# Performance work log

Hardware: AMD Instinct MI355X
Metric: run time of the kernel (lower is better)

Reference implementation:

```python
import jax, jax.numpy as jnp
import numpy as np

D_MODEL = 768
N_HEADS = 12
D_K = D_MODEL // N_HEADS
BATCH = 1
SEQ = 4096


def setup_inputs() -> dict:
    key = jax.random.key(0)
    kx, kq, kk, kv, ko = jax.random.split(key, 5)
    s = 1.0 / np.sqrt(D_MODEL)
    return {
        "x": jax.random.normal(kx, (BATCH, SEQ, D_MODEL), dtype=jnp.float32),
        "wq": jax.random.normal(kq, (D_MODEL, D_MODEL), dtype=jnp.float32) * s,
        "wk": jax.random.normal(kk, (D_MODEL, D_MODEL), dtype=jnp.float32) * s,
        "wv": jax.random.normal(kv, (D_MODEL, D_MODEL), dtype=jnp.float32) * s,
        "wo": jax.random.normal(ko, (D_MODEL, D_MODEL), dtype=jnp.float32) * s,
    }


def reference(x, wq, wk, wv, wo):
    B, S, D = x.shape
    H, dk = N_HEADS, D_K
    # nn.Linear(x) = x @ W.T ; reshape to [B,H,S,dk]
    def proj(w):
        return (x @ w.T).reshape(B, S, H, dk).transpose(0, 2, 1, 3)
    q, k, v = proj(wq), proj(wk), proj(wv)
    scores = jnp.einsum('bhqd,bhkd->bhqk', q, k) / np.sqrt(dk).astype(np.float32)
    attn = jax.nn.softmax(scores, axis=-1)
    out = jnp.einsum('bhqk,bhkd->bhqd', attn, v)
    out = out.transpose(0, 2, 1, 3).reshape(B, S, D)
    return out @ wo.T
```

## Files before the change

### kernel.cpp

```cpp
#include <hip/hip_runtime.h>
#include <stdint.h>

#define SEQ 4096
#define DMODEL 768
#define NHEADS 12
#define DKH 64

typedef __attribute__((ext_vector_type(8))) short short8;
typedef __attribute__((ext_vector_type(4))) float floatx4;

__device__ __forceinline__ unsigned short f2bf(float f) {
    unsigned int u = __float_as_uint(f);
    u += 0x7fffu + ((u >> 16) & 1u);
    return (unsigned short)(u >> 16);
}

__device__ __forceinline__ float exp2fast(float x) {
    return __builtin_amdgcn_exp2f(x);
}

__device__ __forceinline__ unsigned int cvt_pk_bf16(float lo, float hi) {
    unsigned int r;
    asm("v_cvt_pk_bf16_f32 %0, %1, %2" : "=v"(r) : "v"(lo), "v"(hi));
    return r;
}

__device__ __forceinline__ int swz(int row, int colb) {
    return colb ^ ((row & 7) << 4);
}

__device__ __forceinline__ void async_copy16(void* lds, const void* g) {
    __builtin_amdgcn_global_load_lds(
        (const __attribute__((address_space(1))) void*)g,
        (__attribute__((address_space(3))) void*)lds,
        16, 0, 0);
}

__global__ __launch_bounds__(256) void castk(const float* __restrict__ src,
                                             unsigned short* __restrict__ dst,
                                             int n4) {
    int i = blockIdx.x * 256 + threadIdx.x;
    if (i >= n4) return;
    float4 v = ((const float4*)src)[i];
    ushort4 o;
    o.x = f2bf(v.x); o.y = f2bf(v.y); o.z = f2bf(v.z); o.w = f2bf(v.w);
    ((ushort4*)dst)[i] = o;
}

template <int MODE>
__global__ __launch_bounds__(256, 2)
void gemm_bt(const unsigned short* __restrict__ A,
             const unsigned short* __restrict__ B,
             void* __restrict__ Out, int K, float scale) {
    __shared__ __align__(128) char smem[(128 * 64 + 64 * 64) * 2];
    char* As = smem;
    char* Bs = smem + 16384;

    const int t = threadIdx.x;
    const int wid = t >> 6, lane = t & 63;
    const int lr = lane & 15, lg = lane >> 4;
    const int wr = wid >> 1, wc = wid & 1;
    const int rowBase = blockIdx.x * 128;
    const int colBase = blockIdx.y * 64;

    const floatx4 zero4 = {0.f, 0.f, 0.f, 0.f};
    floatx4 acc[4][2];
#pragma unroll
    for (int m = 0; m < 4; m++)
#pragma unroll
        for (int n = 0; n < 2; n++) acc[m][n] = zero4;

    for (int kb = 0; kb < K; kb += 64) {
        __syncthreads();
#pragma unroll
        for (int i = 0; i < 4; i++) {
            int o = i * 4096 + t * 16;
            int row = o >> 7, colb = o & 127;
            const char* src = (const char*)A + ((size_t)(rowBase + row) * K + kb) * 2 + swz(row, colb);
            async_copy16(As + i * 4096 + wid * 1024, src);
        }
#pragma unroll
        for (int i = 0; i < 2; i++) {
            int o = i * 4096 + t * 16;
            int row = o >> 7, colb = o & 127;
            const char* src = (const char*)B + ((size_t)(colBase + row) * K + kb) * 2 + swz(row, colb);
            async_copy16(Bs + i * 4096 + wid * 1024, src);
        }
        __syncthreads();

        short8 a[4][2], b[2][2];
#pragma unroll
        for (int m = 0; m < 4; m++)
#pragma unroll
            for (int kk = 0; kk < 2; kk++) {
                int row = wr * 64 + m * 16 + lr;
                int colb = kk * 64 + lg * 16;
                a[m][kk] = *(const short8*)(As + row * 128 + swz(row, colb));
            }
#pragma unroll
        for (int n = 0; n < 2; n++)
#pragma unroll
            for (int kk = 0; kk < 2; kk++) {
                int row = wc * 32 + n * 16 + lr;
                int colb = kk * 64 + lg * 16;
                b[n][kk] = *(const short8*)(Bs + row * 128 + swz(row, colb));
            }
#pragma unroll
        for (int m = 0; m < 4; m++)
#pragma unroll
            for (int n = 0; n < 2; n++)
#pragma unroll
                for (int kk = 0; kk < 2; kk++)
                    acc[m][n] = __builtin_amdgcn_mfma_f32_16x16x32_bf16(
                        a[m][kk], b[n][kk], acc[m][n], 0, 0, 0);
    }

#pragma unroll
    for (int m = 0; m < 4; m++)
#pragma unroll
        for (int n = 0; n < 2; n++) {
            if (MODE == 2) {
                int srow0 = rowBase + wr * 64 + m * 16 + lg * 4;
                int z = srow0 & 31;
                int pos0 = (srow0 & ~31) + 8 * ((z >> 2) & 3) + 4 * (z >> 4);
                int col = colBase + wc * 32 + n * 16 + lr;
                ushort4 o4;
                o4.x = f2bf(acc[m][n][0] * scale);
                o4.y = f2bf(acc[m][n][1] * scale);
                o4.z = f2bf(acc[m][n][2] * scale);
                o4.w = f2bf(acc[m][n][3] * scale);
                *(ushort4*)((unsigned short*)Out + (size_t)col * SEQ + pos0) = o4;
            } else {
#pragma unroll
                for (int r = 0; r < 4; r++) {
                    int srow = rowBase + wr * 64 + m * 16 + lg * 4 + r;
                    int col = colBase + wc * 32 + n * 16 + lr;
                    float v = acc[m][n][r] * scale;
                    if (MODE == 0) {
                        int h = col >> 6, d = col & 63;
                        ((unsigned short*)Out)[((size_t)h * SEQ + srow) * DKH + d] = f2bf(v);
                    } else {
                        ((float*)Out)[(size_t)srow * DMODEL + col] = v;
                    }
                }
            }
        }
}

__global__ __launch_bounds__(256, 4)
void attn_k(const unsigned short* __restrict__ Q,
            const unsigned short* __restrict__ Kp,
            const unsigned short* __restrict__ Vt,
            unsigned short* __restrict__ AO) {
    __shared__ __align__(128) char smem[32768];
    char* Ks = smem;
    char* Vs = smem + 16384;

    const int t = threadIdx.x;
    const int wid = t >> 6, lane = t & 63;
    const int lr = lane & 15, lg = lane >> 4;

    const int h = blockIdx.y, qb = blockIdx.x;
    const size_t headOff = (size_t)h * SEQ * DKH;

    const unsigned short* qptr = Q + headOff + (size_t)(qb * 64 + wid * 16 + lr) * DKH + lg * 8;
    short8 qf[2];
    qf[0] = *(const short8*)qptr;
    qf[1] = *(const short8*)(qptr + 32);

    const short8 ones8 = {(short)0x3F80, (short)0x3F80, (short)0x3F80, (short)0x3F80,
                          (short)0x3F80, (short)0x3F80, (short)0x3F80, (short)0x3F80};
    const floatx4 zero4 = {0.f, 0.f, 0.f, 0.f};
    float mrun = -3.0e38f;
    floatx4 acc[4];
    floatx4 acc_l = zero4;
#pragma unroll
    for (int f = 0; f < 4; f++) acc[f] = zero4;

    for (int kv = 0; kv < SEQ; kv += 128) {
        __syncthreads();
#pragma unroll
        for (int i = 0; i < 4; i++) {
            int o = i * 4096 + t * 16;
            int row = o >> 7, colb = o & 127;
            const char* src = (const char*)(Kp + headOff + (size_t)(kv + row) * DKH) + swz(row, colb);
            async_copy16(Ks + i * 4096 + wid * 1024, src);
        }
#pragma unroll
        for (int i = 0; i < 4; i++) {
            int o = i * 4096 + t * 16;
            int row = o >> 8, colb = o & 255;
            const char* src = (const char*)(Vt + (size_t)(h * DKH + row) * SEQ + kv) + swz(row, colb);
            async_copy16(Vs + i * 4096 + wid * 1024, src);
        }
        __syncthreads();

        floatx4 s[8];
#pragma unroll
        for (int ct = 0; ct < 8; ct++) s[ct] = zero4;
#pragma unroll
        for (int ct = 0; ct < 8; ct++)
#pragma unroll
            for (int kk = 0; kk < 2; kk++) {
                int row = ct * 16 + lr;
                int colb = kk * 64 + lg * 16;
                short8 kf = *(const short8*)(Ks + row * 128 + swz(row, colb));
                s[ct] = __builtin_amdgcn_mfma_f32_16x16x32_bf16(kf, qf[kk], s[ct], 0, 0, 0);
            }

        float mt = s[0][0];
#pragma unroll
        for (int ct = 0; ct < 8; ct++)
            mt = fmaxf(fmaxf(fmaxf(mt, s[ct][0]), fmaxf(s[ct][1], s[ct][2])), s[ct][3]);
        mt = fmaxf(mt, __shfl_xor(mt, 16));
        mt = fmaxf(mt, __shfl_xor(mt, 32));
        if (!__all(mt <= mrun + 8.0f)) {
            float mnew = fmaxf(mrun, mt);
            float al = exp2fast(mrun - mnew);
#pragma unroll
            for (int f = 0; f < 4; f++)
#pragma unroll
                for (int r = 0; r < 4; r++) acc[f][r] *= al;
            acc_l[0] *= al;
            mrun = mnew;
        }
#pragma unroll
        for (int ct = 0; ct < 8; ct++)
#pragma unroll
            for (int r = 0; r < 4; r++) s[ct][r] = exp2fast(s[ct][r] - mrun);

#pragma unroll
        for (int kk = 0; kk < 4; kk++) {
            uint4 pw;
            pw.x = cvt_pk_bf16(s[2 * kk][0], s[2 * kk][1]);
            pw.y = cvt_pk_bf16(s[2 * kk][2], s[2 * kk][3]);
            pw.z = cvt_pk_bf16(s[2 * kk + 1][0], s[2 * kk + 1][1]);
            pw.w = cvt_pk_bf16(s[2 * kk + 1][2], s[2 * kk + 1][3]);
            short8 pf = *(const short8*)&pw;
#pragma unroll
            for (int f = 0; f < 4; f++) {
                int row = f * 16 + lr;
                int byteo = row * 256 + kk * 64 + lg * 16;
                byteo ^= (row & 7) << 4;
                short8 vf = *(const short8*)(Vs + byteo);
                acc[f] = __builtin_amdgcn_mfma_f32_16x16x32_bf16(vf, pf, acc[f], 0, 0, 0);
            }
            acc_l = __builtin_amdgcn_mfma_f32_16x16x32_bf16(ones8, pf, acc_l, 0, 0, 0);
        }
    }

    float inv = 1.0f / acc_l[0];
    int srow = qb * 64 + wid * 16 + lr;
#pragma unroll
    for (int f = 0; f < 4; f++) {
        ushort4 o4;
        o4.x = f2bf(acc[f][0] * inv);
        o4.y = f2bf(acc[f][1] * inv);
        o4.z = f2bf(acc[f][2] * inv);
        o4.w = f2bf(acc[f][3] * inv);
        int col = h * DKH + f * 16 + lg * 4;
        *(ushort4*)(AO + (size_t)srow * DMODEL + col) = o4;
    }
}

extern "C" void kernel_launch(void* const* d_in, const int* in_sizes, int n_in,
                              void* d_out, int out_size, void* d_ws, size_t ws_size,
                              hipStream_t stream) {
    const float* x  = (const float*)d_in[0];
    const float* wq = (const float*)d_in[1];
    const float* wk = (const float*)d_in[2];
    const float* wv = (const float*)d_in[3];
    const float* wo = (const float*)d_in[4];

    char* ws = (char*)d_ws;
    unsigned short* xb  = (unsigned short*)(ws + 0);
    unsigned short* wqb = (unsigned short*)(ws + 6291456);
    unsigned short* wkb = (unsigned short*)(ws + 7471104);
    unsigned short* wvb = (unsigned short*)(ws + 8650752);
    unsigned short* wob = (unsigned short*)(ws + 9830400);
    unsigned short* Qb  = (unsigned short*)(ws + 11010048);
    unsigned short* Kb  = (unsigned short*)(ws + 17301504);
    unsigned short* VTb = (unsigned short*)(ws + 23592960);
    unsigned short* AOb = (unsigned short*)(ws + 29884416);

    castk<<<3072, 256, 0, stream>>>(x, xb, 786432);
    castk<<<576, 256, 0, stream>>>(wq, wqb, 147456);
    castk<<<576, 256, 0, stream>>>(wk, wkb, 147456);
    castk<<<576, 256, 0, stream>>>(wv, wvb, 147456);
    castk<<<576, 256, 0, stream>>>(wo, wob, 147456);

    dim3 g(32, 12);
    gemm_bt<0><<<g, 256, 0, stream>>>(xb, wqb, Qb, DMODEL, 0.18033688f);
    gemm_bt<0><<<g, 256, 0, stream>>>(xb, wkb, Kb, DMODEL, 1.0f);
    gemm_bt<2><<<g, 256, 0, stream>>>(xb, wvb, VTb, DMODEL, 1.0f);

    attn_k<<<dim3(64, 12), 256, 0, stream>>>(Qb, Kb, VTb, AOb);

    gemm_bt<1><<<g, 256, 0, stream>>>(AOb, wob, d_out, DMODEL, 1.0f);
}
```

Measured before the change: 140.5 us.

## Fuse weight casts and QKV GEMMs, pipeline GEMM and attention loads

Four weight-cast launches become one, and the three QKV projection GEMMs become a single launch with a 36-wide grid. Both GEMM kernels now double-buffer their LDS tiles with explicit vmcnt waits so global loads overlap MFMA work. The attention kernel moves from 128-wide to 64-wide KV tiles with a three-stage LDS ring buffer, and remaps block IDs to change the order in which blocks cover heads. These changes aim to cut launch overhead and memory stalls, at the cost of more LDS per block (48KB), which could lower occupancy.

```diff
diff --git a/kernel.cpp b/kernel.cpp
--- a/kernel.cpp
+++ b/kernel.cpp
@@ -47,14 +47,139 @@
     ((ushort4*)dst)[i] = o;
 }
 
-template <int MODE>
+__global__ __launch_bounds__(256) void castw(const float* __restrict__ w0,
+                                             const float* __restrict__ w1,
+                                             const float* __restrict__ w2,
+                                             const float* __restrict__ w3,
+                                             unsigned short* __restrict__ dst) {
+    int b = blockIdx.x;
+    int wsel = b / 576;
+    int i = (b % 576) * 256 + threadIdx.x;
+    const float* src = (wsel == 0) ? w0 : (wsel == 1) ? w1 : (wsel == 2) ? w2 : w3;
+    float4 v = ((const float4*)src)[i];
+    ushort4 o;
+    o.x = f2bf(v.x); o.y = f2bf(v.y); o.z = f2bf(v.z); o.w = f2bf(v.w);
+    ((ushort4*)(dst + (size_t)wsel * 589824))[i] = o;
+}
+
+#define STAGE_G(bsel, kb)                                                              \
+    do {                                                                               \
+        char* As_ = smem + (bsel) * 24576;                                             \
+        _Pragma("unroll") for (int ii = 0; ii < 4; ii++) {                             \
+            int o = ii * 4096 + t * 16;                                                \
+            int row = o >> 7, colb = o & 127;                                          \
+            async_copy16(As_ + ii * 4096 + wid * 1024,                                 \
+                         (const char*)A + ((size_t)(rowBase + row) * DMODEL + (kb)) * 2 \
+                             + swz(row, colb));                                        \
+        }                                                                              \
+        _Pragma("unroll") for (int ii = 0; ii < 2; ii++) {                             \
+            int o = ii * 4096 + t * 16;                                                \
+            int row = o >> 7, colb = o & 127;                                          \
+            async_copy16(As_ + 16384 + ii * 4096 + wid * 1024,                         \
+                         (const char*)B + ((size_t)(colBase + row) * DMODEL + (kb)) * 2 \
+                             + swz(row, colb));                                        \
+        }                                                                              \
+    } while (0)
+
+#define GEMM_COMPUTE(As, Bs)                                                           \
+    do {                                                                               \
+        short8 a_[4][2], b_[2][2];                                                     \
+        _Pragma("unroll") for (int m = 0; m < 4; m++)                                  \
+            _Pragma("unroll") for (int kk = 0; kk < 2; kk++) {                         \
+                int row = wr * 64 + m * 16 + lr;                                       \
+                int colb = kk * 64 + lg * 16;                                          \
+                a_[m][kk] = *(const short8*)((As) + row * 128 + swz(row, colb));       \
+            }                                                                          \
+        _Pragma("unroll") for (int n = 0; n < 2; n++)                                  \
+            _Pragma("unroll") for (int kk = 0; kk < 2; kk++) {                         \
+                int row = wc * 32 + n * 16 + lr;                                       \
+                int colb = kk * 64 + lg * 16;                                          \
+                b_[n][kk] = *(const short8*)((Bs) + row * 128 + swz(row, colb));       \
+            }                                                                          \
+        _Pragma("unroll") for (int m = 0; m < 4; m++)                                  \
+            _Pragma("unroll") for (int n = 0; n < 2; n++)                              \
+                _Pragma("unroll") for (int kk = 0; kk < 2; kk++)                       \
+                    acc[m][n] = __builtin_amdgcn_mfma_f32_16x16x32_bf16(               \
+                        a_[m][kk], b_[n][kk], acc[m][n], 0, 0, 0);                     \
+    } while (0)
+
 __global__ __launch_bounds__(256, 2)
-void gemm_bt(const unsigned short* __restrict__ A,
-             const unsigned short* __restrict__ B,
-             void* __restrict__ Out, int K, float scale) {
-    __shared__ __align__(128) char smem[(128 * 64 + 64 * 64) * 2];
-    char* As = smem;
-    char* Bs = smem + 16384;
+void gemm_qkv(const unsigned short* __restrict__ A,
+              const unsigned short* __restrict__ W,
+              unsigned short* __restrict__ OutBase, float qscale) {
+    __shared__ __align__(128) char smem[49152];
+
+    const int t = threadIdx.x;
+    const int wid = t >> 6, lane = t & 63;
+    const int lr = lane & 15, lg = lane >> 4;
+    const int wr = wid >> 1, wc = wid & 1;
+    const int rowBase = blockIdx.x * 128;
+    const int proj = blockIdx.y / 12;
+    const int colBase = (blockIdx.y % 12) * 64;
+    const unsigned short* B = W + (size_t)proj * 589824;
+
+    const floatx4 zero4 = {0.f, 0.f, 0.f, 0.f};
+    floatx4 acc[4][2];
+#pragma unroll
+    for (int m = 0; m < 4; m++)
+#pragma unroll
+        for (int n = 0; n < 2; n++) acc[m][n] = zero4;
+
+    STAGE_G(0, 0);
+    for (int i = 0; i < 12; ++i) {
+        __builtin_amdgcn_s_barrier();
+        __builtin_amdgcn_sched_barrier(0);
+        if (i < 11) {
+            STAGE_G((i + 1) & 1, (i + 1) * 64);
+            asm volatile("s_waitcnt vmcnt(6)" ::: "memory");
+        } else {
+            asm volatile("s_waitcnt vmcnt(0)" ::: "memory");
+        }
+        __builtin_amdgcn_s_barrier();
+        __builtin_amdgcn_sched_barrier(0);
+        char* As = smem + (i & 1) * 24576;
+        GEMM_COMPUTE(As, As + 16384);
+    }
+
+    if (proj < 2) {
+        unsigned short* O = OutBase + (size_t)proj * 3145728;
+        float scale = (proj == 0) ? qscale : 1.0f;
+#pragma unroll
+        for (int m = 0; m < 4; m++)
+#pragma unroll
+            for (int n = 0; n < 2; n++)
+#pragma unroll
+                for (int r = 0; r < 4; r++) {
+                    int srow = rowBase + wr * 64 + m * 16 + lg * 4 + r;
+                    int col = colBase + wc * 32 + n * 16 + lr;
+                    int h = col >> 6, d = col & 63;
+                    O[((size_t)h * SEQ + srow) * DKH + d] = f2bf(acc[m][n][r] * scale);
+                }
+    } else {
+        unsigned short* O = OutBase + 6291456;
+#pragma unroll
+        for (int m = 0; m < 4; m++)
+#pragma unroll
+            for (int n = 0; n < 2; n++) {
+                int srow0 = rowBase + wr * 64 + m * 16 + lg * 4;
+                int z = srow0 & 31;
+                int pos0 = (srow0 & ~31) + 8 * ((z >> 2) & 3) + 4 * (z >> 4);
+                int col = colBase + wc * 32 + n * 16 + lr;
+                ushort4 o4;
+                o4.x = f2bf(acc[m][n][0]);
+                o4.y = f2bf(acc[m][n][1]);
+                o4.z = f2bf(acc[m][n][2]);
+                o4.w = f2bf(acc[m][n][3]);
+                *(ushort4*)(O + (size_t)col * SEQ + pos0) = o4;
+            }
+    }
+}
+
+__global__ __launch_bounds__(256, 2)
+void gemm_o(const unsigned short* __restrict__ A,
+            const unsigned short* __restrict__ B,
+            float* __restrict__ Out) {
+    __shared__ __align__(128) char smem[49152];
 
     const int t = threadIdx.x;
     const int wid = t >> 6, lane = t & 63;
@@ -70,97 +195,66 @@
 #pragma unroll
         for (int n = 0; n < 2; n++) acc[m][n] = zero4;
 
-    for (int kb = 0; kb < K; kb += 64) {
-        __syncthreads();
-#pragma unroll
-        for (int i = 0; i < 4; i++) {
-            int o = i * 4096 + t * 16;
-            int row = o >> 7, colb = o & 127;
-            const char* src = (const char*)A + ((size_t)(rowBase + row) * K + kb) * 2 + swz(row, colb);
-            async_copy16(As + i * 4096 + wid * 1024, src);
-        }
-#pragma unroll
-        for (int i = 0; i < 2; i++) {
-            int o = i * 4096 + t * 16;
-            int row = o >> 7, colb = o & 127;
-            const char* src = (const char*)B + ((size_t)(colBase + row) * K + kb) * 2 + swz(row, colb);
-            async_copy16(Bs + i * 4096 + wid * 1024, src);
-        }
-        __syncthreads();
-
-        short8 a[4][2], b[2][2];
-#pragma unroll
-        for (int m = 0; m < 4; m++)
-#pragma unroll
-            for (int kk = 0; kk < 2; kk++) {
-                int row = wr * 64 + m * 16 + lr;
-                int colb = kk * 64 + lg * 16;
-                a[m][kk] = *(const short8*)(As + row * 128 + swz(row, colb));
+    STAGE_G(0, 0);
+    for (int i = 0; i < 12; ++i) {
+        __builtin_amdgcn_s_barrier();
+        __builtin_amdgcn_sched_barrier(0);
+        if (i < 11) {
+            STAGE_G((i + 1) & 1, (i + 1) * 64);
+            asm volatile("s_waitcnt vmcnt(6)" ::: "memory");
+        } else {
+            asm volatile("s_waitcnt vmcnt(0)" ::: "memory");
+        }
+        __builtin_amdgcn_s_barrier();
+        __builtin_amdgcn_sched_barrier(0);
+        char* As = smem + (i & 1) * 24576;
+        GEMM_COMPUTE(As, As + 16384);
+    }
+
+#pragma unroll
+    for (int m = 0; m < 4; m++)
+#pragma unroll
+        for (int n = 0; n < 2; n++)
+#pragma unroll
+            for (int r = 0; r < 4; r++) {
+                int srow = rowBase + wr * 64 + m * 16 + lg * 4 + r;
+                int col = colBase + wc * 32 + n * 16 + lr;
+                Out[(size_t)srow * DMODEL + col] = acc[m][n][r];
             }
-#pragma unroll
-        for (int n = 0; n < 2; n++)
-#pragma unroll
-            for (int kk = 0; kk < 2; kk++) {
-                int row = wc * 32 + n * 16 + lr;
-                int colb = kk * 64 + lg * 16;
-                b[n][kk] = *(const short8*)(Bs + row * 128 + swz(row, colb));
-            }
-#pragma unroll
-        for (int m = 0; m < 4; m++)
-#pragma unroll
-            for (int n = 0; n < 2; n++)
-#pragma unroll
-                for (int kk = 0; kk < 2; kk++)
-                    acc[m][n] = __builtin_amdgcn_mfma_f32_16x16x32_bf16(
-                        a[m][kk], b[n][kk], acc[m][n], 0, 0, 0);
-    }
-
-#pragma unroll
-    for (int m = 0; m < 4; m++)
-#pragma unroll
-        for (int n = 0; n < 2; n++) {
-            if (MODE == 2) {
-                int srow0 = rowBase + wr * 64 + m * 16 + lg * 4;
-                int z = srow0 & 31;
-                int pos0 = (srow0 & ~31) + 8 * ((z >> 2) & 3) + 4 * (z >> 4);
-                int col = colBase + wc * 32 + n * 16 + lr;
-                ushort4 o4;
-                o4.x = f2bf(acc[m][n][0] * scale);
-                o4.y = f2bf(acc[m][n][1] * scale);
-                o4.z = f2bf(acc[m][n][2] * scale);
-                o4.w = f2bf(acc[m][n][3] * scale);
-                *(ushort4*)((unsigned short*)Out + (size_t)col * SEQ + pos0) = o4;
-            } else {
-#pragma unroll
-                for (int r = 0; r < 4; r++) {
-                    int srow = rowBase + wr * 64 + m * 16 + lg * 4 + r;
-                    int col = colBase + wc * 32 + n * 16 + lr;
-                    float v = acc[m][n][r] * scale;
-                    if (MODE == 0) {
-                        int h = col >> 6, d = col & 63;
-                        ((unsigned short*)Out)[((size_t)h * SEQ + srow) * DKH + d] = f2bf(v);
-                    } else {
-                        ((float*)Out)[(size_t)srow * DMODEL + col] = v;
-                    }
-                }
-            }
-        }
-}
+}
+
+#define STAGE_A(bsel, kv0)                                                             \
+    do {                                                                               \
+        char* Kd_ = smem + (bsel) * 16384;                                             \
+        _Pragma("unroll") for (int ii = 0; ii < 2; ii++) {                             \
+            int o = ii * 4096 + t * 16;                                                \
+            int row = o >> 7, colb = o & 127;                                          \
+            async_copy16(Kd_ + ii * 4096 + wid * 1024,                                 \
+                         (const char*)(Kp + headOff + (size_t)((kv0) + row) * DKH)     \
+                             + swz(row, colb));                                        \
+        }                                                                              \
+        _Pragma("unroll") for (int ii = 0; ii < 2; ii++) {                             \
+            int o = ii * 4096 + t * 16;                                                \
+            int row = o >> 7, colb = o & 127;                                          \
+            async_copy16(Kd_ + 8192 + ii * 4096 + wid * 1024,                          \
+                         (const char*)(Vt + (size_t)(h * DKH + row) * SEQ + (kv0))     \
+                             + swz(row, colb));                                        \
+        }                                                                              \
+    } while (0)
 
 __global__ __launch_bounds__(256, 4)
 void attn_k(const unsigned short* __restrict__ Q,
             const unsigned short* __restrict__ Kp,
             const unsigned short* __restrict__ Vt,
             unsigned short* __restrict__ AO) {
-    __shared__ __align__(128) char smem[32768];
-    char* Ks = smem;
-    char* Vs = smem + 16384;
+    __shared__ __align__(128) char smem[49152];
 
     const int t = threadIdx.x;
     const int wid = t >> 6, lane = t & 63;
     const int lr = lane & 15, lg = lane >> 4;
 
-    const int h = blockIdx.y, qb = blockIdx.x;
+    int nid = (blockIdx.x & 7) * 96 + (blockIdx.x >> 3);
+    const int h = nid >> 6, qb = nid & 63;
     const size_t headOff = (size_t)h * SEQ * DKH;
 
     const unsigned short* qptr = Q + headOff + (size_t)(qb * 64 + wid * 16 + lr) * DKH + lg * 8;
@@ -177,29 +271,27 @@
 #pragma unroll
     for (int f = 0; f < 4; f++) acc[f] = zero4;
 
-    for (int kv = 0; kv < SEQ; kv += 128) {
-        __syncthreads();
-#pragma unroll
-        for (int i = 0; i < 4; i++) {
-            int o = i * 4096 + t * 16;
-            int row = o >> 7, colb = o & 127;
-            const char* src = (const char*)(Kp + headOff + (size_t)(kv + row) * DKH) + swz(row, colb);
-            async_copy16(Ks + i * 4096 + wid * 1024, src);
-        }
-#pragma unroll
-        for (int i = 0; i < 4; i++) {
-            int o = i * 4096 + t * 16;
-            int row = o >> 8, colb = o & 255;
-            const char* src = (const char*)(Vt + (size_t)(h * DKH + row) * SEQ + kv) + swz(row, colb);
-            async_copy16(Vs + i * 4096 + wid * 1024, src);
-        }
-        __syncthreads();
-
-        floatx4 s[8];
-#pragma unroll
-        for (int ct = 0; ct < 8; ct++) s[ct] = zero4;
-#pragma unroll
-        for (int ct = 0; ct < 8; ct++)
+    STAGE_A(0, 0);
+    STAGE_A(1, 64);
+
+    int cA = 0;
+    for (int tt = 0; tt < 64; ++tt) {
+        if (tt < 62) asm volatile("s_waitcnt vmcnt(4)" ::: "memory");
+        else         asm volatile("s_waitcnt vmcnt(0)" ::: "memory");
+        __builtin_amdgcn_s_barrier();
+        __builtin_amdgcn_sched_barrier(0);
+        if (tt < 62) {
+            int cC = cA + 2; if (cC >= 3) cC -= 3;
+            STAGE_A(cC, (tt + 2) * 64);
+        }
+        char* Ks = smem + cA * 16384;
+        char* Vs = Ks + 8192;
+
+        floatx4 s[4];
+#pragma unroll
+        for (int ct = 0; ct < 4; ct++) s[ct] = zero4;
+#pragma unroll
+        for (int ct = 0; ct < 4; ct++)
 #pragma unroll
             for (int kk = 0; kk < 2; kk++) {
                 int row = ct * 16 + lr;
@@ -210,7 +302,7 @@
 
         float mt = s[0][0];
 #pragma unroll
-        for (int ct = 0; ct < 8; ct++)
+        for (int ct = 0; ct < 4; ct++)
             mt = fmaxf(fmaxf(fmaxf(mt, s[ct][0]), fmaxf(s[ct][1], s[ct][2])), s[ct][3]);
         mt = fmaxf(mt, __shfl_xor(mt, 16));
         mt = fmaxf(mt, __shfl_xor(mt, 32));
@@ -225,12 +317,12 @@
             mrun = mnew;
         }
 #pragma unroll
-        for (int ct = 0; ct < 8; ct++)
+        for (int ct = 0; ct < 4; ct++)
 #pragma unroll
             for (int r = 0; r < 4; r++) s[ct][r] = exp2fast(s[ct][r] - mrun);
 
 #pragma unroll
-        for (int kk = 0; kk < 4; kk++) {
+        for (int kk = 0; kk < 2; kk++) {
             uint4 pw;
             pw.x = cvt_pk_bf16(s[2 * kk][0], s[2 * kk][1]);
             pw.y = cvt_pk_bf16(s[2 * kk][2], s[2 * kk][3]);
@@ -240,13 +332,14 @@
 #pragma unroll
             for (int f = 0; f < 4; f++) {
                 int row = f * 16 + lr;
-                int byteo = row * 256 + kk * 64 + lg * 16;
-                byteo ^= (row & 7) << 4;
+                int byteo = (row * 128 + kk * 64 + lg * 16) ^ ((row & 7) << 4);
                 short8 vf = *(const short8*)(Vs + byteo);
                 acc[f] = __builtin_amdgcn_mfma_f32_16x16x32_bf16(vf, pf, acc[f], 0, 0, 0);
             }
             acc_l = __builtin_amdgcn_mfma_f32_16x16x32_bf16(ones8, pf, acc_l, 0, 0, 0);
         }
+
+        cA = (cA == 2) ? 0 : cA + 1;
     }
 
     float inv = 1.0f / acc_l[0];
@@ -275,8 +368,6 @@
     char* ws = (char*)d_ws;
     unsigned short* xb  = (unsigned short*)(ws + 0);
     unsigned short* wqb = (unsigned short*)(ws + 6291456);
-    unsigned short* wkb = (unsigned short*)(ws + 7471104);
-    unsigned short* wvb = (unsigned short*)(ws + 8650752);
     unsigned short* wob = (unsigned short*)(ws + 9830400);
     unsigned short* Qb  = (unsigned short*)(ws + 11010048);
     unsigned short* Kb  = (unsigned short*)(ws + 17301504);
@@ -284,17 +375,11 @@
     unsigned short* AOb = (unsigned short*)(ws + 29884416);
 
     castk<<<3072, 256, 0, stream>>>(x, xb, 786432);
-    castk<<<576, 256, 0, stream>>>(wq, wqb, 147456);
-    castk<<<576, 256, 0, stream>>>(wk, wkb, 147456);
-    castk<<<576, 256, 0, stream>>>(wv, wvb, 147456);
-    castk<<<576, 256, 0, stream>>>(wo, wob, 147456);
-
-    dim3 g(32, 12);
-    gemm_bt<0><<<g, 256, 0, stream>>>(xb, wqb, Qb, DMODEL, 0.18033688f);
-    gemm_bt<0><<<g, 256, 0, stream>>>(xb, wkb, Kb, DMODEL, 1.0f);
-    gemm_bt<2><<<g, 256, 0, stream>>>(xb, wvb, VTb, DMODEL, 1.0f);
-
-    attn_k<<<dim3(64, 12), 256, 0, stream>>>(Qb, Kb, VTb, AOb);
-
-    gemm_bt<1><<<g, 256, 0, stream>>>(AOb, wob, d_out, DMODEL, 1.0f);
-}
+    castw<<<2304, 256, 0, stream>>>(wq, wk, wv, wo, wqb);
+
+    gemm_qkv<<<dim3(32, 36), 256, 0, stream>>>(xb, wqb, Qb, 0.18033688f);
+
+    attn_k<<<dim3(768), 256, 0, stream>>>(Qb, Kb, VTb, AOb);
+
+    gemm_o<<<dim3(32, 12), 256, 0, stream>>>(AOb, wob, (float*)d_out);
+}
```

After: 132.8 us. 1.06x faster.
